# Optimization experiments

Measured on AMD Instinct MI355X. Metric: run time of the kernel, lower is better.

## Reference

```python
import jax, jax.numpy as jnp
import numpy as np

B, DIM, H, W = 2, 512, 48, 48
HEADS = 8
HD = DIM // HEADS
NS = 7
R = NS // 2
SCALE = HD ** -0.5
EPS = 1e-12


def _proj(x, w, b):
    # 1x1 conv == channel linear: x [B,C,H,W], w [O,C], b [O]
    return jnp.einsum('bchw,oc->bohw', x, w) + b[None, :, None, None]


def _to_heads(t):
    # [B,C,H,W] -> [B,heads,H,W,head_dim]
    return t.reshape(B, HEADS, HD, H, W).transpose(0, 1, 3, 4, 2)


def setup_inputs() -> dict:
    key = jax.random.key(0)
    ks = jax.random.split(key, 9)
    std = DIM ** -0.5
    inp = {'x': jax.random.normal(ks[0], (B, DIM, H, W), jnp.float32)}
    names = ['wq', 'bq', 'wk', 'bk', 'wv', 'bv', 'wo', 'bo']
    for i, n in enumerate(names):
        if n.startswith('w'):
            inp[n] = jax.random.normal(ks[i + 1], (DIM, DIM), jnp.float32) * std
        else:
            inp[n] = jnp.zeros((DIM,), jnp.float32)
    return inp


def reference(x, wq, bq, wk, bk, wv, bv, wo, bo):
    q = _proj(x, wq, bq)
    k = _proj(x, wk, bk)
    v = _proj(x, wv, bv)
    qh, kh, vh = _to_heads(q), _to_heads(k), _to_heads(v)

    offs = jnp.arange(-R, R + 1)
    oy, ox = jnp.meshgrid(offs, offs, indexing='ij')
    oy, ox = oy.reshape(-1), ox.reshape(-1)  # [K]
    by, bx = jnp.meshgrid(jnp.arange(H), jnp.arange(W), indexing='ij')
    ny = by[..., None] + oy  # [H,W,K]
    nx = bx[..., None] + ox
    valid = (ny >= 0) & (ny < H) & (nx >= 0) & (nx < W)  # [H,W,K]
    ny = jnp.clip(ny, 0, H - 1)
    nx = jnp.clip(nx, 0, W - 1)

    K = NS * NS
    T = H * W
    # gather neighborhoods: [B,heads,H,W,K,head_dim]
    k_nb = kh[:, :, ny, nx].reshape(B, HEADS, T, K, HD)
    v_nb = vh[:, :, ny, nx].reshape(B, HEADS, T, K, HD)
    q_tok = qh.reshape(B, HEADS, T, HD)

    scores = jnp.einsum('bhtd,bhtkd->bhtk', q_tok, k_nb) * SCALE
    neg = jnp.finfo(scores.dtype).min
    scores = jnp.where(valid.reshape(1, 1, T, K), scores, neg)
    attn = jax.nn.softmax(scores, axis=-1)
    out = jnp.einsum('bhtk,bhtkd->bhtd', attn, v_nb)

    # exclude self-value component (self-attention path)
    sv = vh.reshape(B, HEADS, T, HD)
    sv_unit = sv / jnp.maximum(jnp.linalg.norm(sv, axis=-1, keepdims=True), EPS)
    out = out - (out * sv_unit).sum(-1, keepdims=True) * sv_unit

    # [B,heads,T,HD] -> [B,C,H,W]
    out = out.reshape(B, HEADS, H, W, HD).transpose(0, 1, 4, 2, 3).reshape(B, DIM, H, W)
    return _proj(out, wo, bo)
```

## Files before the change

### kernel.cpp

```cpp
#include <hip/hip_runtime.h>
#include <hip/hip_bf16.h>
#include <math.h>

typedef __hip_bfloat16 bf16;
typedef __attribute__((ext_vector_type(4))) float f32x4;
typedef __attribute__((ext_vector_type(8))) short s16x8;
typedef __attribute__((ext_vector_type(4))) short s16x4;

#define B_     2
#define DIM_   512
#define Hh     48
#define Ww     48
#define T_     2304
#define HEADS_ 8
#define HD_    64
#define NS_    7
#define R_     3
#define KK_    49

typedef __attribute__((address_space(3))) unsigned       lds_u32_t;
typedef __attribute__((address_space(1))) const unsigned glb_u32_t;

__device__ __forceinline__ void gload16(const short* g, short* l) {
    __builtin_amdgcn_global_load_lds((glb_u32_t*)g, (lds_u32_t*)l, 16, 0, 0);
}

__device__ __forceinline__ short f2bs(float f) {
    bf16 h = __float2bfloat16(f);
    return *(short*)&h;
}

__device__ __forceinline__ float bs2f(short s) {
    bf16 h = *reinterpret_cast<const bf16*>(&s);
    return __bfloat162float(h);
}

__device__ __forceinline__ s16x8 cvt8(const float* __restrict__ p) {
    f32x4 a = *(const f32x4*)p;
    f32x4 b = *(const f32x4*)(p + 4);
    s16x8 r;
    r[0] = f2bs(a[0]); r[1] = f2bs(a[1]); r[2] = f2bs(a[2]); r[3] = f2bs(a[3]);
    r[4] = f2bs(b[0]); r[5] = f2bs(b[1]); r[6] = f2bs(b[2]); r[7] = f2bs(b[3]);
    return r;
}

__global__ __launch_bounds__(256) void prep(
    const float* __restrict__ x,
    const float* __restrict__ wq, const float* __restrict__ wk,
    const float* __restrict__ wv, const float* __restrict__ wo,
    bf16* __restrict__ xt, bf16* __restrict__ wb)
{
    __shared__ short tile[64 * 72];
    const int gid = blockIdx.x;
    const int tid = threadIdx.x;

    if (gid < 512) {
        const int i     = gid * 256 + tid;
        const int which = i >> 15;
        const int off   = (i & 32767) * 8;
        const float* src = (which == 0) ? wq : (which == 1) ? wk
                         : (which == 2) ? wv : wo;
        *(s16x8*)((short*)wb + which * 262144 + off) = cvt8(src + off);
        return;
    }

    const int pid = gid - 512;
    const int b   = pid / 288;
    const int rem = pid - b * 288;
    const int t0  = (rem % 36) * 64;
    const int c0  = (rem / 36) * 64;

    const float* X = x + (size_t)b * DIM_ * T_;

    const int c_l = tid >> 4;
    const int t4  = (tid & 15) * 4;
#pragma unroll
    for (int cp = 0; cp < 4; ++cp) {
        const int c = cp * 16 + c_l;
        f32x4 v = *(const f32x4*)(X + (size_t)(c0 + c) * T_ + t0 + t4);
#pragma unroll
        for (int e = 0; e < 4; ++e) tile[(t4 + e) * 72 + c] = f2bs(v[e]);
    }
    __syncthreads();

    const int t_l = tid >> 2;
    const int c16 = (tid & 3) * 16;
    short* dst = (short*)xt + ((size_t)b * T_ + t0 + t_l) * DIM_ + c0 + c16;
    *(s16x8*)(dst)     = *(const s16x8*)(&tile[t_l * 72 + c16]);
    *(s16x8*)(dst + 8) = *(const s16x8*)(&tile[t_l * 72 + c16 + 8]);
}

__global__ __launch_bounds__(256) void gemm_qkv(
    const bf16* __restrict__ xt, const bf16* __restrict__ wb,
    const float* __restrict__ bq, const float* __restrict__ bk,
    const float* __restrict__ bv,
    bf16* __restrict__ qb2, bf16* __restrict__ kb2, bf16* __restrict__ vb2)
{
    const int tt   = blockIdx.x * 128;
    const int ot   = blockIdx.y * 128;
    const int b    = blockIdx.z;
    const int proj = ot >> 9;
    const int orow = ot & 511;
    const int h0   = orow >> 6;

    const float* bsel = (proj == 0) ? bq : (proj == 1) ? bk : bv;
    const short* Wb   = (const short*)wb + proj * 262144;
    const short* X    = (const short*)xt + (size_t)b * T_ * DIM_;
    short*       sel  = (short*)((proj == 0) ? qb2 : (proj == 1) ? kb2 : vb2);

    __shared__ __align__(16) short Xs[128 * 32];
    __shared__ __align__(16) short Ws[128 * 32];

    const int tid  = threadIdx.x;
    const int lane = tid & 63;
    const int wid  = tid >> 6;
    const int ln   = lane & 15;
    const int qq   = lane >> 4;

    const int swz8 = (((lane & 3) ^ ((lane >> 3) & 3)) * 8);
    const int rsw  = (ln >> 1) & 3;

    f32x4 acc[2][8];
#pragma unroll
    for (int r = 0; r < 2; ++r)
#pragma unroll
        for (int n = 0; n < 8; ++n) acc[r][n] = (f32x4){0.f, 0.f, 0.f, 0.f};

    for (int kk = 0; kk < DIM_; kk += 32) {
#pragma unroll
        for (int half = 0; half < 2; ++half) {
            const int r0 = wid * 32 + half * 16;
            const int r  = r0 + (lane >> 2);
            gload16(X  + (size_t)(tt   + r) * DIM_ + kk + swz8, &Xs[r0 * 32]);
            gload16(Wb + (size_t)(orow + r) * DIM_ + kk + swz8, &Ws[r0 * 32]);
        }
        __syncthreads();

        s16x8 a[2];
#pragma unroll
        for (int r = 0; r < 2; ++r) {
            const int rr = r * 64 + wid * 16 + ln;
            a[r] = *(const s16x8*)&Xs[rr * 32 + ((qq ^ rsw) * 8)];
        }
#pragma unroll
        for (int n = 0; n < 8; ++n) {
            const int rw = n * 16 + ln;
            s16x8 bf = *(const s16x8*)&Ws[rw * 32 + ((qq ^ rsw) * 8)];
#pragma unroll
            for (int r = 0; r < 2; ++r)
                acc[r][n] = __builtin_amdgcn_mfma_f32_16x16x32_bf16(a[r], bf, acc[r][n], 0, 0, 0);
        }
        __syncthreads();
    }

    const size_t tb = (size_t)(b * HEADS_ + h0);
#pragma unroll
    for (int r = 0; r < 2; ++r)
#pragma unroll
        for (int n = 0; n < 8; ++n) {
            const int hn   = n >> 2;
            const int d    = (n & 3) * 16 + ln;
            const float bi = bsel[orow + n * 16 + ln];
#pragma unroll
            for (int e = 0; e < 4; ++e) {
                const int t = tt + r * 64 + wid * 16 + (lane >> 4) * 4 + e;
                sel[((tb + hn) * T_ + t) * HD_ + d] = f2bs(acc[r][n][e] + bi);
            }
        }
}

__global__ __launch_bounds__(256) void gemm_out(
    const bf16* __restrict__ ao, const bf16* __restrict__ wb,
    const float* __restrict__ bo, float* __restrict__ out)
{
    const int tt = blockIdx.x * 64;
    const int ot = blockIdx.y * 64;
    const int b  = blockIdx.z;

    const short* X  = (const short*)ao + (size_t)b * T_ * DIM_;
    const short* Wb = (const short*)wb + 3 * 262144;

    __shared__ __align__(16) short Ws[64 * 32];
    __shared__ __align__(16) short Xs[64 * 32];

    const int tid  = threadIdx.x;
    const int lane = tid & 63;
    const int wid  = tid >> 6;
    const int ln   = lane & 15;
    const int qq   = lane >> 4;

    const int swz8 = (((lane & 3) ^ ((lane >> 3) & 3)) * 8);
    const int rsw  = (ln >> 1) & 3;

    f32x4 acc[4];
#pragma unroll
    for (int n = 0; n < 4; ++n) acc[n] = (f32x4){0.f, 0.f, 0.f, 0.f};

    for (int kk = 0; kk < DIM_; kk += 32) {
        {
            const int r0 = wid * 16;
            const int r  = r0 + (lane >> 2);
            gload16(Wb + (size_t)(ot + r) * DIM_ + kk + swz8, &Ws[r0 * 32]);
            gload16(X  + (size_t)(tt + r) * DIM_ + kk + swz8, &Xs[r0 * 32]);
        }
        __syncthreads();

        s16x8 a = *(const s16x8*)&Ws[(wid * 16 + ln) * 32 + ((qq ^ rsw) * 8)];
#pragma unroll
        for (int n = 0; n < 4; ++n) {
            s16x8 bf = *(const s16x8*)&Xs[(n * 16 + ln) * 32 + ((qq ^ rsw) * 8)];
            acc[n] = __builtin_amdgcn_mfma_f32_16x16x32_bf16(a, bf, acc[n], 0, 0, 0);
        }
        __syncthreads();
    }

    float* obase = out + (size_t)b * DIM_ * T_;
#pragma unroll
    for (int n = 0; n < 4; ++n) {
        const int t = tt + n * 16 + ln;
#pragma unroll
        for (int e = 0; e < 4; ++e) {
            const int o    = ot + wid * 16 + (lane >> 4) * 4 + e;
            obase[(size_t)o * T_ + t] = acc[n][e] + bo[o];
        }
    }
}

__global__ __launch_bounds__(256, 4) void attn_mfma(
    const bf16* __restrict__ qb2, const bf16* __restrict__ kb2,
    const bf16* __restrict__ vb2, bf16* __restrict__ ao)
{
    __shared__ __align__(16) char smem[32000];
    short* Kl = (short*)smem;
    short* VT = (short*)smem;
    short* Pl = (short*)(smem + 25600);
    float* Ol = (float*)(smem + 25600);

    const int l   = blockIdx.x;
    const int idx = (l & 7) * 288 + (l >> 3);
    const int bh  = idx / 144;
    const int rem = idx - bh * 144;
    const int y   = rem / 3;
    const int x0  = (rem % 3) * 16;

    const short* qb  = (const short*)qb2 + (size_t)bh * T_ * HD_;
    const short* kb  = (const short*)kb2 + (size_t)bh * T_ * HD_;
    const short* vbb = (const short*)vb2 + (size_t)bh * T_ * HD_;

    const int tid  = threadIdx.x;
    const int lane = tid & 63;
    const int wv   = tid >> 6;
    const int qq   = lane >> 4;
    const int ln   = lane & 15;

    if (tid < 32) {
        const int t = tid >> 1, c = tid & 1;
        *(s16x8*)&Pl[t * 200 + 176 + c * 8] = (s16x8){0,0,0,0,0,0,0,0};
    }
    {
        const int swc = (((lane & 7) ^ (lane >> 3)) & 7) * 8;
#pragma unroll
        for (int p = 0; p < 6; ++p) {
            const int g = p * 4 + wv;
            if (g < 21) {
                const int r  = g * 8 + (lane >> 3);
                const int wy = r / 24, u = r - wy * 24;
                const int gy = min(max(y + wy - 3, 0), 47);
                const int gx = min(max(x0 + u - 3, 0), 47);
                gload16(kb + (size_t)(gy * 48 + gx) * 64 + swc, &Kl[g * 8 * 64]);
            }
        }
    }
    s16x8 qreg0, qreg1;
    {
        const short* qp = qb + (size_t)(y * 48 + x0 + ln) * 64 + qq * 8;
        qreg0 = *(const s16x8*)(qp);
        qreg1 = *(const s16x8*)(qp + 32);
    }
    s16x4 vreg[10];
    {
        const int rr0 = tid >> 4;
        const int d4  = (tid & 15) * 4;
#pragma unroll
        for (int p = 0; p < 10; ++p) {
            const int rr = p * 16 + rr0;
            if (rr < 154) {
                const int wy = rr / 22, u = rr - wy * 22;
                const int gy = min(max(y + wy - 3, 0), 47);
                const int gx = min(max(x0 + u - 3, 0), 47);
                vreg[p] = *(const s16x4*)(vbb + (size_t)(gy * 48 + gx) * 64 + d4);
            }
        }
    }
    __syncthreads();

    f32x4 acc[11];
#pragma unroll
    for (int mt = 0; mt < 11; ++mt) acc[mt] = (f32x4){0.f, 0.f, 0.f, 0.f};
    __builtin_amdgcn_s_setprio(1);
#pragma unroll
    for (int ks = 0; ks < 2; ++ks) {
        s16x8 bq_ = (ks == 0) ? qreg0 : qreg1;
#pragma unroll
        for (int mt = 0; mt < 11; ++mt) {
            const int rr = mt * 16 + ln;
            s16x8 ak = *(const s16x8*)&Kl[rr * 64 + (((ks * 4 + qq) ^ (ln & 7)) * 8)];
            acc[mt] = __builtin_amdgcn_mfma_f32_16x16x32_bf16(ak, bq_, acc[mt], 0, 0, 0);
        }
    }
    __builtin_amdgcn_s_setprio(0);

    const int dx = ln;
    float mxv = -3.0e38f;
#pragma unroll
    for (int mt = 0; mt < 11; ++mt) {
#pragma unroll
        for (int e = 0; e < 4; ++e) {
            const int w  = mt * 16 + qq * 4 + e;
            const int wy = w / 24, u = w - wy * 24;
            const bool valid = (w < 168) &&
                               ((unsigned)(u - dx) <= 6u) &&
                               ((unsigned)(y + wy - 3) < 48u) &&
                               ((unsigned)(x0 + u - 3) < 48u);
            const float s = valid ? acc[mt][e] * 0.125f : -3.0e38f;
            acc[mt][e] = s;
            mxv = fmaxf(mxv, s);
        }
    }
    mxv = fmaxf(mxv, __shfl_xor(mxv, 16));
    mxv = fmaxf(mxv, __shfl_xor(mxv, 32));
    float sum = 0.f;
#pragma unroll
    for (int mt = 0; mt < 11; ++mt)
#pragma unroll
        for (int e = 0; e < 4; ++e) {
            const float p = __expf(acc[mt][e] - mxv);
            acc[mt][e] = p;
            sum += p;
        }
    sum += __shfl_xor(sum, 16);
    sum += __shfl_xor(sum, 32);
    const float inv = 1.0f / sum;

#pragma unroll
    for (int mt = 0; mt < 11; ++mt) {
        const int owner = (mt >= 9) ? 3 : (mt / 3);
        if (wv == owner) {
#pragma unroll
            for (int e = 0; e < 4; ++e) {
                const int w = mt * 16 + qq * 4 + e;
                Pl[ln * 200 + w] = f2bs(acc[mt][e] * inv);
            }
        }
    }
    __syncthreads();

    {
        const int d = tid >> 2, c = tid & 3;
        *(s16x8*)&VT[d * 200 + 168 + c * 8] = (s16x8){0,0,0,0,0,0,0,0};
    }
#pragma unroll
    for (int pp = 0; pp < 2; ++pp) {
        const int r2 = pp * 256 + tid;
        if (r2 < 448) {
            const int wy = r2 >> 6, d = r2 & 63;
            *(unsigned*)&VT[d * 200 + wy * 24 + 22] = 0u;
        }
    }
    {
        const int rr0 = tid >> 4;
        const int d4  = (tid & 15) * 4;
        const int rot = tid & 3;
#pragma unroll
        for (int p = 0; p < 10; ++p) {
            const int rr = p * 16 + rr0;
            if (rr < 154) {
                const int wy = rr / 22, u = rr - wy * 22;
                const int w  = wy * 24 + u;
#pragma unroll
                for (int e = 0; e < 4; ++e) {
                    const int ee = (e + rot) & 3;
                    VT[(d4 + ee) * 200 + w] = vreg[p][ee];
                }
            }
        }
    }
    __syncthreads();

    f32x4 oacc = (f32x4){0.f, 0.f, 0.f, 0.f};
    __builtin_amdgcn_s_setprio(1);
#pragma unroll
    for (int ks = 0; ks < 6; ++ks) {
        s16x8 ap  = *(const s16x8*)&Pl[ln * 200 + ks * 32 + qq * 8];
        s16x8 bv_ = *(const s16x8*)&VT[(wv * 16 + ln) * 200 + ks * 32 + qq * 8];
        oacc = __builtin_amdgcn_mfma_f32_16x16x32_bf16(ap, bv_, oacc, 0, 0, 0);
    }
    __builtin_amdgcn_s_setprio(0);
    __syncthreads();
#pragma unroll
    for (int e = 0; e < 4; ++e)
        Ol[(qq * 4 + e) * 72 + wv * 16 + ln] = oacc[e];
    __syncthreads();

    {
        const int tt = tid >> 4;
        const int dl = tid & 15;
        const int tg = y * 48 + x0 + tt;
        const float o0 = Ol[tt * 72 + dl],      o1 = Ol[tt * 72 + dl + 16],
                    o2 = Ol[tt * 72 + dl + 32], o3 = Ol[tt * 72 + dl + 48];
        const short* vs = vbb + (size_t)tg * 64 + dl;
        const float v0 = bs2f(vs[0]),  v1 = bs2f(vs[16]),
                    v2 = bs2f(vs[32]), v3 = bs2f(vs[48]);
        float n2  = v0 * v0 + v1 * v1 + v2 * v2 + v3 * v3;
        float odv = o0 * v0 + o1 * v1 + o2 * v2 + o3 * v3;
#pragma unroll
        for (int off = 1; off < 16; off <<= 1) {
            n2  += __shfl_xor(n2, off);
            odv += __shfl_xor(odv, off);
        }
        const float mxn = fmaxf(sqrtf(n2), 1e-12f);
        const float cf  = odv / (mxn * mxn);
        const int b = bh >> 3, h = bh & 7;
        bf16* dst = ao + ((size_t)b * T_ + tg) * DIM_ + h * 64 + dl;
        dst[0]  = __float2bfloat16(o0 - cf * v0);
        dst[16] = __float2bfloat16(o1 - cf * v1);
        dst[32] = __float2bfloat16(o2 - cf * v2);
        dst[48] = __float2bfloat16(o3 - cf * v3);
    }
}

extern "C" void kernel_launch(void* const* d_in, const int* in_sizes, int n_in,
                              void* d_out, int out_size, void* d_ws, size_t ws_size,
                              hipStream_t stream)
{
    (void)in_sizes; (void)n_in; (void)out_size; (void)ws_size;

    const float* x  = (const float*)d_in[0];
    const float* wq = (const float*)d_in[1];
    const float* bq = (const float*)d_in[2];
    const float* wk = (const float*)d_in[3];
    const float* bk = (const float*)d_in[4];
    const float* wv = (const float*)d_in[5];
    const float* bv = (const float*)d_in[6];
    const float* wo = (const float*)d_in[7];
    const float* bo = (const float*)d_in[8];
    float* out = (float*)d_out;

    const size_t per = (size_t)B_ * HEADS_ * T_ * HD_;
    bf16* qb2 = (bf16*)d_ws;
    bf16* kb2 = qb2 + per;
    bf16* vb2 = kb2 + per;
    bf16* xa  = vb2 + per;
    bf16* wb  = xa + per;

    prep<<<dim3(512 + 576), 256, 0, stream>>>(x, wq, wk, wv, wo, xa, wb);

    dim3 g1(T_ / 128, 1536 / 128, B_);
    gemm_qkv<<<g1, 256, 0, stream>>>(xa, wb, bq, bk, bv, qb2, kb2, vb2);

    attn_mfma<<<dim3(B_ * HEADS_ * (T_ / 16)), 256, 0, stream>>>(qb2, kb2, vb2, xa);

    dim3 g2(T_ / 64, DIM_ / 64, B_);
    gemm_out<<<g2, 256, 0, stream>>>(xa, wb, bo, out);
}
```

Measured before the change: 59.64 us.

## Double-buffer LDS tiles in QKV and output projection GEMMs

Both projection GEMMs now keep two LDS buffers per operand and issue the global-to-LDS loads for the next K tile before computing on the current one. This drops one barrier per iteration and lets memory traffic overlap the MFMA work. In exchange it doubles shared memory per block, which could reduce occupancy, and overlap is still limited by the barrier that waits on outstanding loads.

```diff
diff --git a/kernel.cpp b/kernel.cpp
--- a/kernel.cpp
+++ b/kernel.cpp
@@ -108,8 +108,8 @@
     const short* X    = (const short*)xt + (size_t)b * T_ * DIM_;
     short*       sel  = (short*)((proj == 0) ? qb2 : (proj == 1) ? kb2 : vb2);
 
-    __shared__ __align__(16) short Xs[128 * 32];
-    __shared__ __align__(16) short Ws[128 * 32];
+    __shared__ __align__(16) short Xs[2][128 * 32];
+    __shared__ __align__(16) short Ws[2][128 * 32];
 
     const int tid  = threadIdx.x;
     const int lane = tid & 63;
@@ -119,6 +119,7 @@
 
     const int swz8 = (((lane & 3) ^ ((lane >> 3) & 3)) * 8);
     const int rsw  = (ln >> 1) & 3;
+    const int rst  = (lane >> 2);
 
     f32x4 acc[2][8];
 #pragma unroll
@@ -126,26 +127,37 @@
 #pragma unroll
         for (int n = 0; n < 8; ++n) acc[r][n] = (f32x4){0.f, 0.f, 0.f, 0.f};
 
-    for (int kk = 0; kk < DIM_; kk += 32) {
-#pragma unroll
-        for (int half = 0; half < 2; ++half) {
-            const int r0 = wid * 32 + half * 16;
-            const int r  = r0 + (lane >> 2);
-            gload16(X  + (size_t)(tt   + r) * DIM_ + kk + swz8, &Xs[r0 * 32]);
-            gload16(Wb + (size_t)(orow + r) * DIM_ + kk + swz8, &Ws[r0 * 32]);
-        }
-        __syncthreads();
-
+#pragma unroll
+    for (int half = 0; half < 2; ++half) {
+        const int r0 = wid * 32 + half * 16;
+        const int r  = r0 + rst;
+        gload16(X  + (size_t)(tt   + r) * DIM_ + 0 + swz8, &Xs[0][r0 * 32]);
+        gload16(Wb + (size_t)(orow + r) * DIM_ + 0 + swz8, &Ws[0][r0 * 32]);
+    }
+    __syncthreads();
+
+    for (int k = 0; k < 16; ++k) {
+        const int cur = k & 1;
+        if (k < 15) {
+            const int kk = (k + 1) * 32;
+#pragma unroll
+            for (int half = 0; half < 2; ++half) {
+                const int r0 = wid * 32 + half * 16;
+                const int r  = r0 + rst;
+                gload16(X  + (size_t)(tt   + r) * DIM_ + kk + swz8, &Xs[cur ^ 1][r0 * 32]);
+                gload16(Wb + (size_t)(orow + r) * DIM_ + kk + swz8, &Ws[cur ^ 1][r0 * 32]);
+            }
+        }
         s16x8 a[2];
 #pragma unroll
         for (int r = 0; r < 2; ++r) {
             const int rr = r * 64 + wid * 16 + ln;
-            a[r] = *(const s16x8*)&Xs[rr * 32 + ((qq ^ rsw) * 8)];
+            a[r] = *(const s16x8*)&Xs[cur][rr * 32 + ((qq ^ rsw) * 8)];
         }
 #pragma unroll
         for (int n = 0; n < 8; ++n) {
             const int rw = n * 16 + ln;
-            s16x8 bf = *(const s16x8*)&Ws[rw * 32 + ((qq ^ rsw) * 8)];
+            s16x8 bf = *(const s16x8*)&Ws[cur][rw * 32 + ((qq ^ rsw) * 8)];
 #pragma unroll
             for (int r = 0; r < 2; ++r)
                 acc[r][n] = __builtin_amdgcn_mfma_f32_16x16x32_bf16(a[r], bf, acc[r][n], 0, 0, 0);
@@ -180,8 +192,8 @@
     const short* X  = (const short*)ao + (size_t)b * T_ * DIM_;
     const short* Wb = (const short*)wb + 3 * 262144;
 
-    __shared__ __align__(16) short Ws[64 * 32];
-    __shared__ __align__(16) short Xs[64 * 32];
+    __shared__ __align__(16) short Ws[2][64 * 32];
+    __shared__ __align__(16) short Xs[2][64 * 32];
 
     const int tid  = threadIdx.x;
     const int lane = tid & 63;
@@ -191,24 +203,33 @@
 
     const int swz8 = (((lane & 3) ^ ((lane >> 3) & 3)) * 8);
     const int rsw  = (ln >> 1) & 3;
+    const int rst  = (lane >> 2);
 
     f32x4 acc[4];
 #pragma unroll
     for (int n = 0; n < 4; ++n) acc[n] = (f32x4){0.f, 0.f, 0.f, 0.f};
 
-    for (int kk = 0; kk < DIM_; kk += 32) {
-        {
+    {
+        const int r0 = wid * 16;
+        const int r  = r0 + rst;
+        gload16(Wb + (size_t)(ot + r) * DIM_ + 0 + swz8, &Ws[0][r0 * 32]);
+        gload16(X  + (size_t)(tt + r) * DIM_ + 0 + swz8, &Xs[0][r0 * 32]);
+    }
+    __syncthreads();
+
+    for (int k = 0; k < 16; ++k) {
+        const int cur = k & 1;
+        if (k < 15) {
+            const int kk = (k + 1) * 32;
             const int r0 = wid * 16;
-            const int r  = r0 + (lane >> 2);
-            gload16(Wb + (size_t)(ot + r) * DIM_ + kk + swz8, &Ws[r0 * 32]);
-            gload16(X  + (size_t)(tt + r) * DIM_ + kk + swz8, &Xs[r0 * 32]);
-        }
-        __syncthreads();
-
-        s16x8 a = *(const s16x8*)&Ws[(wid * 16 + ln) * 32 + ((qq ^ rsw) * 8)];
+            const int r  = r0 + rst;
+            gload16(Wb + (size_t)(ot + r) * DIM_ + kk + swz8, &Ws[cur ^ 1][r0 * 32]);
+            gload16(X  + (size_t)(tt + r) * DIM_ + kk + swz8, &Xs[cur ^ 1][r0 * 32]);
+        }
+        s16x8 a = *(const s16x8*)&Ws[cur][(wid * 16 + ln) * 32 + ((qq ^ rsw) * 8)];
 #pragma unroll
         for (int n = 0; n < 4; ++n) {
-            s16x8 bf = *(const s16x8*)&Xs[(n * 16 + ln) * 32 + ((qq ^ rsw) * 8)];
+            s16x8 bf = *(const s16x8*)&Xs[cur][(n * 16 + ln) * 32 + ((qq ^ rsw) * 8)];
             acc[n] = __builtin_amdgcn_mfma_f32_16x16x32_bf16(a, bf, acc[n], 0, 0, 0);
         }
         __syncthreads();
```

After: 62.81 us. 5.3% more time.
